# Kernel tuning notes

Hardware: AMD Instinct MI355X
Metric: run time of the kernel (lower is better)

The kernel has to match this reference:

```python
import jax, jax.numpy as jnp
from jax import lax
import numpy as np

D_MODEL = 256
NQ = 256          # nqueries / npoint
RADIUS = 0.3
NSAMPLE = 16
EPS = 1e-5


def _conv1d(x, W, b):  # x: (B,C,N), W: (O,C)
    return jnp.einsum('bcn,oc->bon', x, W) + b[None, :, None]


def _bn1d(x, g, be):  # train-mode batchnorm over (B, N)
    m = x.mean(axis=(0, 2), keepdims=True)
    v = x.var(axis=(0, 2), keepdims=True)
    return g[None, :, None] * (x - m) * lax.rsqrt(v + EPS) + be[None, :, None]


def _bn2d(x, g, be):  # x: (B,C,Q,S)
    m = x.mean(axis=(0, 2, 3), keepdims=True)
    v = x.var(axis=(0, 2, 3), keepdims=True)
    return g[None, :, None, None] * (x - m) * lax.rsqrt(v + EPS) + be[None, :, None, None]


def _fps(xyz, nq):
    # sequential farthest point sampling, starts at index 0 (matches CUDA impl)
    B, N, _ = xyz.shape

    def step(carry, _):
        dist, far = carry
        centroid = jnp.take_along_axis(xyz, far[:, None, None], axis=1)  # (B,1,3)
        d = jnp.sum((xyz - centroid) ** 2, axis=-1)                      # (B,N)
        dist = jnp.minimum(dist, d)
        nxt = jnp.argmax(dist, axis=-1).astype(jnp.int32)
        return (dist, nxt), far

    init = (jnp.full((B, N), 1e10, xyz.dtype), jnp.zeros((B,), jnp.int32))
    _, inds = lax.scan(step, init, None, length=nq)
    return inds.T  # (B,nq)


def _ball_query(query_xyz, xyz, radius, nsample):
    # query_xyz: (B,Q,3), xyz: (B,N,3) -> idx (B,Q,nsample) int32
    N = xyz.shape[1]
    d2 = jnp.sum((query_xyz[:, :, None, :] - xyz[:, None, :, :]) ** 2, axis=-1)  # (B,Q,N)
    within = d2 < radius * radius
    scores = jnp.where(within, jnp.arange(N, dtype=jnp.int32), jnp.int32(N))
    neg_top, _ = lax.top_k(-scores, nsample)          # nsample smallest scores, in order
    idx = -neg_top                                    # (B,Q,nsample)
    cnt = within.sum(axis=-1)                         # (B,Q)
    first = jnp.where(cnt > 0, idx[..., 0], 0)        # fill value (first neighbor, else 0)
    valid = jnp.arange(nsample) < cnt[..., None]
    return jnp.where(valid, idx, first[..., None])


def setup_inputs() -> dict:
    key = jax.random.key(0)
    ks = jax.random.split(key, 32)
    B, N, C = 16, 4096, D_MODEL
    s = 0.02
    inp = {
        'encode_xyz': jax.random.uniform(ks[0], (B, N, 3), jnp.float32),
        'encode_features': jax.random.normal(ks[1], (B, C, N), jnp.float32),
        # FFN_vote: conv1 -> bn -> relu -> conv2 -> bn -> relu -> conv3
        'W1': jax.random.normal(ks[2], (C, C), jnp.float32) * s,
        'b1': jnp.zeros((C,), jnp.float32),
        'g1': jnp.ones((C,), jnp.float32),
        'be1': jnp.zeros((C,), jnp.float32),
        'W2': jax.random.normal(ks[3], (C, C), jnp.float32) * s,
        'b2': jnp.zeros((C,), jnp.float32),
        'g2': jnp.ones((C,), jnp.float32),
        'be2': jnp.zeros((C,), jnp.float32),
        'W3': jax.random.normal(ks[4], (3 + C, C), jnp.float32) * s,
        'b3': jnp.zeros((3 + C,), jnp.float32),
        # SA module shared MLP (conv2d 1x1): (C+3)->C->C->C, each with BN2d
        'mW1': jax.random.normal(ks[5], (C, C + 3), jnp.float32) * s,
        'mb1': jnp.zeros((C,), jnp.float32),
        'mg1': jnp.ones((C,), jnp.float32),
        'mbe1': jnp.zeros((C,), jnp.float32),
        'mW2': jax.random.normal(ks[6], (C, C), jnp.float32) * s,
        'mb2': jnp.zeros((C,), jnp.float32),
        'mg2': jnp.ones((C,), jnp.float32),
        'mbe2': jnp.zeros((C,), jnp.float32),
        'mW3': jax.random.normal(ks[7], (C, C), jnp.float32) * s,
        'mb3': jnp.zeros((C,), jnp.float32),
        'mg3': jnp.ones((C,), jnp.float32),
        'mbe3': jnp.zeros((C,), jnp.float32),
    }
    return inp


def reference(encode_xyz, encode_features, W1, b1, g1, be1, W2, b2, g2, be2, W3, b3,
              mW1, mb1, mg1, mbe1, mW2, mb2, mg2, mbe2, mW3, mb3, mg3, mbe3):
    B, N, _ = encode_xyz.shape

    # FFN_vote
    h = jax.nn.relu(_bn1d(_conv1d(encode_features, W1, b1), g1, be1))
    h = jax.nn.relu(_bn1d(_conv1d(h, W2, b2), g2, be2))
    out = _conv1d(h, W3, b3)                      # (B, 3+C, N)

    coord_shift = jnp.clip(jax.nn.sigmoid(out[:, :3, :]), 0.1, 0.9)
    vote_xyz = encode_xyz + coord_shift.transpose(0, 2, 1) - 0.5   # (B,N,3)

    feat = encode_features + out[:, 3:, :]
    feat = feat / jnp.linalg.norm(feat, axis=1, keepdims=True)     # L2 normalize over C

    sample_inds = _fps(encode_xyz, NQ)                             # (B,NQ) int32

    # SA module: gather new centers from vote_xyz at FPS inds
    query_xyz = jnp.take_along_axis(vote_xyz, sample_inds[:, :, None], axis=1)  # (B,NQ,3)

    idx = _ball_query(query_xyz, vote_xyz, RADIUS, NSAMPLE)        # (B,NQ,NS)
    bidx = jnp.arange(B)[:, None, None]
    grouped_xyz = (vote_xyz[bidx, idx] - query_xyz[:, :, None, :]) / RADIUS  # (B,NQ,NS,3)
    grouped_feat = feat.transpose(0, 2, 1)[bidx, idx]                         # (B,NQ,NS,C)
    g = jnp.concatenate([grouped_xyz, grouped_feat], axis=-1)                 # (B,NQ,NS,3+C)
    g = g.transpose(0, 3, 1, 2)                                               # (B,3+C,NQ,NS)

    g = jax.nn.relu(_bn2d(jnp.einsum('bcqs,oc->boqs', g, mW1) + mb1[None, :, None, None], mg1, mbe1))
    g = jax.nn.relu(_bn2d(jnp.einsum('bcqs,oc->boqs', g, mW2) + mb2[None, :, None, None], mg2, mbe2))
    g = jax.nn.relu(_bn2d(jnp.einsum('bcqs,oc->boqs', g, mW3) + mb3[None, :, None, None], mg3, mbe3))
    query_features = jnp.max(g, axis=-1)                                      # (B,C,NQ)

    return vote_xyz, encode_xyz, sample_inds, query_xyz, query_features
```

## Files before the change

kernel.cpp:

```cpp
#include <hip/hip_runtime.h>
#include <math.h>

#define NPT 4096
#define NB 16

typedef short v8s __attribute__((ext_vector_type(8)));
typedef float v4f __attribute__((ext_vector_type(4)));

__device__ __forceinline__ float dist2e(float x, float y, float z,
                                        float cx, float cy, float cz) {
    float dx = __fsub_rn(x, cx), dy = __fsub_rn(y, cy), dz = __fsub_rn(z, cz);
    return __fadd_rn(__fadd_rn(__fmul_rn(dx, dx), __fmul_rn(dy, dy)), __fmul_rn(dz, dz));
}

__device__ __forceinline__ unsigned long long packdi(float v, int n) {
    return ((unsigned long long)__float_as_uint(v) << 32) |
           (unsigned long long)(0xFFFFFFFFu - (unsigned)n);
}

__device__ __forceinline__ unsigned short f2bf(float f) {
    unsigned u = __float_as_uint(f);
    u = u + 0x7FFFu + ((u >> 16) & 1u);
    return (unsigned short)(u >> 16);
}

__device__ __forceinline__ unsigned pk2(float a, float b) {
    unsigned r;
    asm("v_cvt_pk_bf16_f32 %0, %1, %2" : "=v"(r) : "v"(a), "v"(b));
    return r;
}

__device__ __forceinline__ uint2 split2(float a, float b) {
    unsigned h = pk2(a, b);
    float ra = __uint_as_float(h << 16);
    float rb = __uint_as_float(h & 0xFFFF0000u);
    unsigned l = pk2(a - ra, b - rb);
    return make_uint2(h, l);
}

__device__ __forceinline__ void bn8(v4f* xv, const float* __restrict__ scl,
                                    const float* __restrict__ sft, int base) {
    const v4f s0 = *(const v4f*)(scl + base);
    const v4f s1 = *(const v4f*)(scl + base + 4);
    const v4f f0 = *(const v4f*)(sft + base);
    const v4f f1 = *(const v4f*)(sft + base + 4);
    #pragma unroll
    for (int i = 0; i < 8; ++i) {
        const float si = (i < 4) ? s0[i] : s1[i - 4];
        const float fi = (i < 4) ? f0[i] : f1[i - 4];
        #pragma unroll
        for (int j = 0; j < 4; ++j)
            xv[i][j] = fmaxf(fmaf(xv[i][j], si, fi), 0.f);
    }
}

template <int CTRL>
__device__ __forceinline__ float dpp_maxf(float v) {
    int o = __builtin_amdgcn_update_dpp(__float_as_int(v), __float_as_int(v),
                                        CTRL, 0xF, 0xF, false);
    return fmaxf(v, __int_as_float(o));
}
template <int CTRL>
__device__ __forceinline__ unsigned dpp_maxu(unsigned v) {
    unsigned o = (unsigned)__builtin_amdgcn_update_dpp((int)v, (int)v,
                                                       CTRL, 0xF, 0xF, false);
    return v > o ? v : o;
}

__device__ void fps_seg(const float* __restrict__ xyz, int b, int it0, int it1,
                        int* __restrict__ inds_i, float* __restrict__ inds_f,
                        float* __restrict__ dws, int* __restrict__ farws,
                        char* scr) {
    unsigned long long (*s_red)[4] = (unsigned long long (*)[4])scr;
    const int t = threadIdx.x;
    const int lane = t & 63, wid = t >> 6;
    const float* pb = xyz + (size_t)b * NPT * 3;
    float px[16], py[16], pz[16], d[16];
    #pragma unroll
    for (int j = 0; j < 16; ++j) {
        int p = j * 256 + t;
        px[j] = pb[p * 3 + 0];
        py[j] = pb[p * 3 + 1];
        pz[j] = pb[p * 3 + 2];
    }
    int far;
    if (it0 == 0) {
        #pragma unroll
        for (int j = 0; j < 16; ++j) d[j] = 1e10f;
        far = 0;
    } else {
        #pragma unroll
        for (int j = 0; j < 16; ++j) d[j] = dws[b * 4096 + j * 256 + t];
        far = farws[b];
    }
    for (int it = it0; it < it1; ++it) {
        const int par = it & 1;
        if (t == 0) { inds_i[it] = far; inds_f[it] = (float)far; }
        const float cx = pb[far * 3 + 0];
        const float cy = pb[far * 3 + 1];
        const float cz = pb[far * 3 + 2];
        d[0] = fminf(d[0], dist2e(px[0], py[0], pz[0], cx, cy, cz));
        unsigned long long best = packdi(d[0], t);
        #pragma unroll
        for (int j = 1; j < 16; ++j) {
            d[j] = fminf(d[j], dist2e(px[j], py[j], pz[j], cx, cy, cz));
            unsigned long long c = packdi(d[j], j * 256 + t);
            if (c > best) best = c;
        }
        const unsigned hi = (unsigned)(best >> 32);
        const unsigned lo = (unsigned)(best & 0xFFFFFFFFull);
        float m = __uint_as_float(hi);
        m = dpp_maxf<0x111>(m);
        m = dpp_maxf<0x112>(m);
        m = dpp_maxf<0x114>(m);
        m = dpp_maxf<0x118>(m);
        m = dpp_maxf<0x142>(m);
        m = dpp_maxf<0x143>(m);
        const unsigned mbits = (unsigned)__builtin_amdgcn_readlane(__float_as_int(m), 63);
        unsigned cand = (hi == mbits) ? lo : 0u;
        cand = dpp_maxu<0x111>(cand);
        cand = dpp_maxu<0x112>(cand);
        cand = dpp_maxu<0x114>(cand);
        cand = dpp_maxu<0x118>(cand);
        cand = dpp_maxu<0x142>(cand);
        cand = dpp_maxu<0x143>(cand);
        const unsigned wlo = (unsigned)__builtin_amdgcn_readlane((int)cand, 63);
        if (lane == 0)
            s_red[par][wid] = ((unsigned long long)mbits << 32) | (unsigned long long)wlo;
        __syncthreads();
        unsigned long long mm = s_red[par][0];
        if (s_red[par][1] > mm) mm = s_red[par][1];
        if (s_red[par][2] > mm) mm = s_red[par][2];
        if (s_red[par][3] > mm) mm = s_red[par][3];
        far = (int)(0xFFFFFFFFu - (unsigned)(mm & 0xFFFFFFFFull));
    }
    if (it1 < 256) {
        #pragma unroll
        for (int j = 0; j < 16; ++j) dws[b * 4096 + j * 256 + t] = d[j];
        if (t == 0) farws[b] = far;
    }
}

template <bool PRE_BN, bool STATS>
__global__ __launch_bounds__(256, 4)
void fgemm_k(const float* __restrict__ X,
             const unsigned short* __restrict__ Wh,
             const unsigned short* __restrict__ Wl,
             const float* __restrict__ bias,
             const float* __restrict__ scl, const float* __restrict__ sft,
             float* __restrict__ Y,
             float* __restrict__ psum, float* __restrict__ psqr,
             const float* __restrict__ xyz, int* __restrict__ sinds,
             float* __restrict__ inds_f, float* __restrict__ fpsd,
             int* __restrict__ fpsfar, int it0, int it1) {
    __shared__ __align__(16) unsigned short sBh[128 * 64];
    __shared__ __align__(16) unsigned short sBl[128 * 64];
    if (blockIdx.x < 16) {
        fps_seg(xyz, blockIdx.x, it0, it1, sinds + blockIdx.x * 256,
                inds_f + blockIdx.x * 256, fpsd, fpsfar, (char*)sBh);
        return;
    }
    int idx = blockIdx.x - 16;
    idx = (idx & 7) * 128 + (idx >> 3);
    const int b = idx >> 6, rem = idx & 63;
    const int nt = rem >> 1;
    const int n0 = nt * 128, o0 = (rem & 1) * 128;
    const int t = threadIdx.x;
    const int w = t >> 6, lane = t & 63;
    const int wm = (w >> 1) * 64, wn = (w & 1) * 64;
    const int lr = lane & 15, lk = lane >> 4;
    char* cBh = (char*)sBh;
    char* cBl = (char*)sBl;

    v4f acc[4][4];
    v4f zz = {0.f, 0.f, 0.f, 0.f};
    #pragma unroll
    for (int i = 0; i < 4; ++i)
        #pragma unroll
        for (int j = 0; j < 4; ++j) acc[i][j] = zz;

    const size_t aoff = (size_t)(o0 + wm + lr) * 256 + lk * 8;
    const unsigned short* pah = Wh + aoff;
    const unsigned short* pal = Wl + aoff;

    const int cblk = t >> 5, nq = t & 31;
    const float* xb = X + ((size_t)b * 256 + cblk * 8) * 4096 + n0 + nq * 4;

    v4f cur[8];
    #pragma unroll
    for (int i = 0; i < 8; ++i)
        cur[i] = *(const v4f*)(xb + (size_t)i * 4096);
    if (PRE_BN) bn8(cur, scl, sft, cblk * 8);

    #pragma unroll
    for (int ks = 0; ks < 4; ++ks) {
        const int k0 = ks * 64;
        __syncthreads();
        #pragma unroll
        for (int j = 0; j < 4; ++j) {
            const int n = nq * 4 + j;
            uint2 p0 = split2(cur[0][j], cur[1][j]);
            uint2 p1 = split2(cur[2][j], cur[3][j]);
            uint2 p2 = split2(cur[4][j], cur[5][j]);
            uint2 p3 = split2(cur[6][j], cur[7][j]);
            uint4 hh, ll;
            hh.x = p0.x; hh.y = p1.x; hh.z = p2.x; hh.w = p3.x;
            ll.x = p0.y; ll.y = p1.y; ll.z = p2.y; ll.w = p3.y;
            const int ad = n * 128 + ((cblk * 16) ^ ((n & 7) << 4));
            *(uint4*)(cBh + ad) = hh;
            *(uint4*)(cBl + ad) = ll;
        }
        __syncthreads();
        if (ks < 3) {
            #pragma unroll
            for (int i = 0; i < 8; ++i)
                cur[i] = *(const v4f*)(xb + (size_t)(k0 + 64 + i) * 4096);
            if (PRE_BN) bn8(cur, scl, sft, k0 + 64 + cblk * 8);
        }
        #pragma unroll
        for (int kb = 0; kb < 2; ++kb) {
            const int koff = kb * 64 + lk * 16;
            const int ka = k0 + kb * 32;
            v8s ahf[4], alf[4], bhf[4], blf[4];
            #pragma unroll
            for (int f = 0; f < 4; ++f) {
                ahf[f] = *(const v8s*)(pah + (size_t)f * 4096 + ka);
                alf[f] = *(const v8s*)(pal + (size_t)f * 4096 + ka);
                const int rn = wn + f * 16 + lr;
                const int bm = rn * 128 + (koff ^ ((rn & 7) << 4));
                bhf[f] = *(const v8s*)(cBh + bm);
                blf[f] = *(const v8s*)(cBl + bm);
            }
            #pragma unroll
            for (int fm = 0; fm < 4; ++fm)
                #pragma unroll
                for (int fn = 0; fn < 4; ++fn) {
                    acc[fm][fn] = __builtin_amdgcn_mfma_f32_16x16x32_bf16(
                        ahf[fm], bhf[fn], acc[fm][fn], 0, 0, 0);
                    acc[fm][fn] = __builtin_amdgcn_mfma_f32_16x16x32_bf16(
                        ahf[fm], blf[fn], acc[fm][fn], 0, 0, 0);
                    acc[fm][fn] = __builtin_amdgcn_mfma_f32_16x16x32_bf16(
                        alf[fm], bhf[fn], acc[fm][fn], 0, 0, 0);
                }
        }
    }

    float* Yb = Y + (size_t)b * 256 * 4096;
    const int gnt = b * 32 + nt;
    #pragma unroll
    for (int fm = 0; fm < 4; ++fm) {
        const int obase = o0 + wm + fm * 16 + lk * 4;
        float bv[4];
        #pragma unroll
        for (int j = 0; j < 4; ++j) bv[j] = bias[obase + j];
        float ssr[4] = {0.f, 0.f, 0.f, 0.f}, qqr[4] = {0.f, 0.f, 0.f, 0.f};
        #pragma unroll
        for (int fn = 0; fn < 4; ++fn) {
            const int gn = n0 + wn + fn * 16 + lr;
            #pragma unroll
            for (int j = 0; j < 4; ++j) {
                const float yv = acc[fm][fn][j] + bv[j];
                Yb[(size_t)(obase + j) * 4096 + gn] = yv;
                ssr[j] += yv; qqr[j] += yv * yv;
            }
        }
        if (STATS) {
            #pragma unroll
            for (int j = 0; j < 4; ++j) {
                #pragma unroll
                for (int off = 1; off < 16; off <<= 1) {
                    ssr[j] += __shfl_xor(ssr[j], off, 64);
                    qqr[j] += __shfl_xor(qqr[j], off, 64);
                }
            }
            if (lr == 0) {
                const int col = gnt * 2 + (w & 1);
                #pragma unroll
                for (int j = 0; j < 4; ++j) {
                    psum[(size_t)(obase + j) * 1024 + col] = ssr[j];
                    psqr[(size_t)(obase + j) * 1024 + col] = qqr[j];
                }
            }
        }
    }
}

__global__ __launch_bounds__(256)
void prepw_k(const float* __restrict__ W1, const float* __restrict__ W2,
             const float* __restrict__ W3, unsigned short* __restrict__ h1,
             unsigned short* __restrict__ l1, unsigned short* __restrict__ h2,
             unsigned short* __restrict__ l2, unsigned short* __restrict__ h3,
             unsigned short* __restrict__ l3) {
    const int o = blockIdx.x & 255, which = blockIdx.x >> 8, t = threadIdx.x;
    float v;
    unsigned short* ph;
    unsigned short* pl;
    if (which == 0) { v = W1[(size_t)o * 256 + t]; ph = h1; pl = l1; }
    else if (which == 1) { v = W2[(size_t)o * 256 + t]; ph = h2; pl = l2; }
    else { v = W3[(size_t)(o + 3) * 256 + t]; ph = h3; pl = l3; }
    unsigned short hu = f2bf(v);
    float rv = v - __uint_as_float((unsigned)hu << 16);
    ph[o * 256 + t] = hu;
    pl[o * 256 + t] = f2bf(rv);
}

__global__ __launch_bounds__(64)
void fin_k(const float* __restrict__ psum, const float* __restrict__ psqr,
           const float* __restrict__ g, const float* __restrict__ be,
           float* __restrict__ scl, float* __restrict__ sft, int npart) {
    const int c = blockIdx.x, t = threadIdx.x;
    const float4* ps = (const float4*)(psum + (size_t)c * 1024);
    const float4* pq = (const float4*)(psqr + (size_t)c * 1024);
    float s = 0.f, q = 0.f;
    for (int r = t; r < (npart >> 2); r += 64) {
        float4 a = ps[r]; s += a.x + a.y + a.z + a.w;
        float4 b2 = pq[r]; q += b2.x + b2.y + b2.z + b2.w;
    }
    #pragma unroll
    for (int sh = 32; sh; sh >>= 1) {
        s += __shfl_down(s, (unsigned)sh, 64);
        q += __shfl_down(q, (unsigned)sh, 64);
    }
    if (t == 0) {
        float mean = s * (1.f / 65536.f);
        float var = q * (1.f / 65536.f) - mean * mean;
        float sc = g[c] / sqrtf(var + 1e-5f);
        scl[c] = sc;
        sft[c] = be[c] - mean * sc;
    }
}

__global__ __launch_bounds__(256)
void prep_k(const float* __restrict__ mW1, const float* __restrict__ mW2,
            const float* __restrict__ mW3, unsigned short* __restrict__ W1p,
            unsigned short* __restrict__ W2p, unsigned short* __restrict__ W3p) {
    const int o = blockIdx.x & 255, which = blockIdx.x >> 8, t = threadIdx.x;
    if (which == 0) {
        W1p[o * 320 + t] = f2bf(mW1[o * 259 + 3 + t]);
        if (t < 64) {
            float v = (t < 3) ? mW1[o * 259 + t] : 0.f;
            W1p[o * 320 + 256 + t] = f2bf(v);
        }
    } else if (which == 1) {
        W2p[o * 256 + t] = f2bf(mW2[o * 256 + t]);
    } else {
        W3p[o * 256 + t] = f2bf(mW3[o * 256 + t]);
    }
}

__global__ __launch_bounds__(256)
void votefeat_k(const float* __restrict__ OUT, const float* __restrict__ Y2,
                const float* __restrict__ xyz, const float* __restrict__ feats,
                const float* __restrict__ scl2, const float* __restrict__ sft2,
                const float* __restrict__ W3, const float* __restrict__ b3,
                float* __restrict__ vote_out, float* __restrict__ xyz_out,
                unsigned short* __restrict__ featT,
                int* __restrict__ sinds, float* __restrict__ inds_f,
                float* __restrict__ fpsd, int* __restrict__ fpsfar,
                int it0, int it1) {
    __shared__ float tile[32 * 257];
    __shared__ float ssb[32 * 9];
    __shared__ float rn[32];
    __shared__ float sW3[768];
    __shared__ float dred[3][8][33];
    if (blockIdx.x < 16) {
        fps_seg(xyz, blockIdx.x, it0, it1, sinds + blockIdx.x * 256,
                inds_f + blockIdx.x * 256, fpsd, fpsfar, (char*)tile);
        return;
    }
    const int blk = blockIdx.x - 16;
    const int b = blk >> 7, n0 = (blk & 127) * 32;
    const int t = threadIdx.x;
    const int nl = t & 31, co = t >> 5;
    const float* Ob = OUT + (size_t)b * 256 * NPT;
    const float* Yb = Y2 + (size_t)b * 256 * NPT;
    #pragma unroll
    for (int r = 0; r < 3; ++r) sW3[r * 256 + t] = W3[r * 256 + t];
    __syncthreads();
    float ss = 0.f, d0 = 0.f, d1 = 0.f, d2 = 0.f;
    #pragma unroll 4
    for (int ci = 0; ci < 32; ++ci) {
        const int c = ci * 8 + co;
        const size_t coff = (size_t)c * NPT + n0 + nl;
        float v = feats[(size_t)b * 256 * NPT + coff] + Ob[coff];
        tile[nl * 257 + c] = v;
        ss += v * v;
        float h = fmaxf(fmaf(Yb[coff], scl2[c], sft2[c]), 0.f);
        d0 = fmaf(h, sW3[c], d0);
        d1 = fmaf(h, sW3[256 + c], d1);
        d2 = fmaf(h, sW3[512 + c], d2);
    }
    ssb[nl * 9 + co] = ss;
    dred[0][co][nl] = d0;
    dred[1][co][nl] = d1;
    dred[2][co][nl] = d2;
    __syncthreads();
    if (t < 32) {
        float s = 0.f;
        #pragma unroll
        for (int j = 0; j < 8; ++j) s += ssb[t * 9 + j];
        rn[t] = 1.0f / sqrtf(s);
    }
    __syncthreads();
    for (int p = 0; p < 32; ++p)
        featT[((size_t)b * NPT + n0 + p) * 256 + t] = f2bf(tile[p * 257 + t] * rn[p]);
    if (t < 96) {
        const int r = t >> 5, p = t & 31;
        float d = b3[r];
        #pragma unroll
        for (int j = 0; j < 8; ++j) d += dred[r][j][p];
        float sig = 1.f / (1.f + expf(-d));
        sig = fminf(fmaxf(sig, 0.1f), 0.9f);
        const size_t gi = ((size_t)b * NPT + n0 + p) * 3 + r;
        const float e = xyz[gi];
        vote_out[gi] = e + sig - 0.5f;
        xyz_out[gi] = e;
    }
}

__global__ __launch_bounds__(64)
void bq_k(const float* __restrict__ vote, const int* __restrict__ sinds,
          float* __restrict__ qxyz_out, int* __restrict__ idx_out) {
    const int bq = blockIdx.x;
    const int b = bq >> 8;
    const int lane = threadIdx.x;
    __shared__ int s_idx[16];
    const int si = sinds[bq];
    const float* vb = vote + (size_t)b * NPT * 3;
    const float qx = vb[si * 3 + 0], qy = vb[si * 3 + 1], qz = vb[si * 3 + 2];
    if (lane < 3) qxyz_out[bq * 3 + lane] = vb[si * 3 + lane];
    int cnt = 0;
    for (int cb = 0; cb < 64 && cnt < 16; ++cb) {
        int n = cb * 64 + lane;
        float x = vb[n * 3], y = vb[n * 3 + 1], z = vb[n * 3 + 2];
        float d2 = dist2e(x, y, z, qx, qy, qz);
        unsigned long long m = __ballot(d2 < 0.09f);
        while (m && cnt < 16) {
            int bit = __builtin_ctzll(m);
            s_idx[cnt] = cb * 64 + bit;
            ++cnt;
            m &= m - 1;
        }
    }
    __syncthreads();
    if (lane < 16) {
        int v = (lane < cnt) ? s_idx[lane] : (cnt > 0 ? s_idx[0] : 0);
        idx_out[bq * 16 + lane] = v;
    }
}

__global__ __launch_bounds__(256)
void group_k(const unsigned short* __restrict__ featT, const float* __restrict__ vote,
             const float* __restrict__ qxyz, const int* __restrict__ idxs,
             unsigned short* __restrict__ Gt) {
    const int bq = blockIdx.x;
    const int b = bq >> 8, q = bq & 255;
    const int t = threadIdx.x;
    __shared__ int s_i[16];
    __shared__ float s_q[3];
    if (t < 16) s_i[t] = idxs[bq * 16 + t];
    if (t < 3) s_q[t] = qxyz[bq * 3 + t];
    __syncthreads();
    const int s = t >> 4, part = t & 15;
    const int i = s_i[s];
    const size_t nrow = (size_t)b * 4096 + q * 16 + s;
    const uint4* src = (const uint4*)(featT + ((size_t)b * NPT + i) * 256 + part * 16);
    uint4* dst = (uint4*)(Gt + nrow * 320 + part * 16);
    dst[0] = src[0];
    dst[1] = src[1];
    for (int c = 259 + part; c < 320; c += 16) Gt[nrow * 320 + c] = 0;
    if (part < 3) {
        float v = (vote[((size_t)b * NPT + i) * 3 + part] - s_q[part]) * (1.f / 0.3f);
        Gt[nrow * 320 + 256 + part] = f2bf(v);
    }
}

__device__ __forceinline__ unsigned bnpair(unsigned u, float sl, float sh,
                                           float fl, float fh) {
    float lo = __uint_as_float(u << 16);
    float hi = __uint_as_float(u & 0xFFFF0000u);
    lo = fmaxf(fmaf(lo, sl, fl), 0.f);
    hi = fmaxf(fmaf(hi, sh, fh), 0.f);
    unsigned r;
    asm("v_cvt_pk_bf16_f32 %0, %1, %2" : "=v"(r) : "v"(lo), "v"(hi));
    return r;
}

template <int KPAD, bool BNSTAGE, bool EPIMAX>
__global__ __launch_bounds__(256, 2)
void mgemm_k(const unsigned short* __restrict__ Wb,
             const unsigned short* __restrict__ Xt,
             const float* __restrict__ bias,
             const float* __restrict__ scl, const float* __restrict__ sft,
             unsigned short* __restrict__ Yt, float* __restrict__ rmax,
             float* __restrict__ psum, float* __restrict__ psqr) {
    __shared__ __align__(16) unsigned short sA[128 * 64];
    __shared__ __align__(16) unsigned short sB[128 * 64];
    char* cA = (char*)sA;
    char* cB = (char*)sB;
    const int t = threadIdx.x;
    const int n0 = blockIdx.x * 128, o0 = blockIdx.y * 128;
    const int w = t >> 6, lane = t & 63;
    const int wm = (w >> 1) * 64, wn = (w & 1) * 64;
    const int lr = lane & 15, lk = lane >> 4;

    v4f acc[4][4];
    v4f zz = {0.f, 0.f, 0.f, 0.f};
    #pragma unroll
    for (int i = 0; i < 4; ++i)
        #pragma unroll
        for (int j = 0; j < 4; ++j) acc[i][j] = zz;

    const int ra = t >> 1, kc = (t & 1) * 32;
    const unsigned short* asrc = Wb + (size_t)(o0 + ra) * KPAD + kc;
    const unsigned short* bsrc = Xt + (size_t)(n0 + ra) * KPAD + kc;
    constexpr int nk = KPAD / 64;

    uint4 av[4], bv[4];
    #pragma unroll
    for (int i = 0; i < 4; ++i) av[i] = *(const uint4*)(asrc + 8 * i);
    #pragma unroll
    for (int i = 0; i < 4; ++i) bv[i] = *(const uint4*)(bsrc + 8 * i);
    if constexpr (BNSTAGE) {
        #pragma unroll
        for (int i = 0; i < 4; ++i) {
            const int kk = kc + 8 * i;
            float4 s0 = *(const float4*)(scl + kk);
            float4 s1 = *(const float4*)(scl + kk + 4);
            float4 f0 = *(const float4*)(sft + kk);
            float4 f1 = *(const float4*)(sft + kk + 4);
            bv[i].x = bnpair(bv[i].x, s0.x, s0.y, f0.x, f0.y);
            bv[i].y = bnpair(bv[i].y, s0.z, s0.w, f0.z, f0.w);
            bv[i].z = bnpair(bv[i].z, s1.x, s1.y, f1.x, f1.y);
            bv[i].w = bnpair(bv[i].w, s1.z, s1.w, f1.z, f1.w);
        }
    }

    #pragma unroll
    for (int ks = 0; ks < nk; ++ks) {
        __syncthreads();
        #pragma unroll
        for (int i = 0; i < 4; ++i) {
            const int kb2 = (kc + 8 * i) * 2;
            *(uint4*)(cA + ra * 128 + (kb2 ^ ((ra & 7) << 4))) = av[i];
            *(uint4*)(cB + ra * 128 + (kb2 ^ ((ra & 7) << 4))) = bv[i];
        }
        __syncthreads();
        if (ks + 1 < nk) {
            const int k1 = (ks + 1) * 64;
            #pragma unroll
            for (int i = 0; i < 4; ++i) av[i] = *(const uint4*)(asrc + k1 + 8 * i);
            #pragma unroll
            for (int i = 0; i < 4; ++i) bv[i] = *(const uint4*)(bsrc + k1 + 8 * i);
            if constexpr (BNSTAGE) {
                #pragma unroll
                for (int i = 0; i < 4; ++i) {
                    const int kk = k1 + kc + 8 * i;
                    float4 s0 = *(const float4*)(scl + kk);
                    float4 s1 = *(const float4*)(scl + kk + 4);
                    float4 f0 = *(const float4*)(sft + kk);
                    float4 f1 = *(const float4*)(sft + kk + 4);
                    bv[i].x = bnpair(bv[i].x, s0.x, s0.y, f0.x, f0.y);
                    bv[i].y = bnpair(bv[i].y, s0.z, s0.w, f0.z, f0.w);
                    bv[i].z = bnpair(bv[i].z, s1.x, s1.y, f1.x, f1.y);
                    bv[i].w = bnpair(bv[i].w, s1.z, s1.w, f1.z, f1.w);
                }
            }
        }
        #pragma unroll
        for (int kb = 0; kb < 2; ++kb) {
            const int koff = (kb * 32 + lk * 8) * 2;
            v8s af[4], bf[4];
            #pragma unroll
            for (int f = 0; f < 4; ++f) {
                const int rm = wm + f * 16 + lr;
                af[f] = *(const v8s*)(cA + rm * 128 + (koff ^ ((rm & 7) << 4)));
                const int rn = wn + f * 16 + lr;
                bf[f] = *(const v8s*)(cB + rn * 128 + (koff ^ ((rn & 7) << 4)));
            }
            #pragma unroll
            for (int fm = 0; fm < 4; ++fm)
                #pragma unroll
                for (int fn = 0; fn < 4; ++fn)
                    acc[fm][fn] = __builtin_amdgcn_mfma_f32_16x16x32_bf16(
                        af[fm], bf[fn], acc[fm][fn], 0, 0, 0);
        }
    }

    const int bx = blockIdx.x;
    #pragma unroll
    for (int fm = 0; fm < 4; ++fm) {
        const int obase = o0 + wm + fm * 16 + lk * 4;
        const float4 bv4 = *(const float4*)(bias + obase);
        float s0 = 0.f, s1 = 0.f, s2 = 0.f, s3 = 0.f;
        float q0 = 0.f, q1 = 0.f, q2 = 0.f, q3 = 0.f;
        #pragma unroll
        for (int fn = 0; fn < 4; ++fn) {
            float y0 = acc[fm][fn][0] + bv4.x;
            float y1 = acc[fm][fn][1] + bv4.y;
            float y2 = acc[fm][fn][2] + bv4.z;
            float y3 = acc[fm][fn][3] + bv4.w;
            s0 += y0; s1 += y1; s2 += y2; s3 += y3;
            q0 += y0 * y0; q1 += y1 * y1; q2 += y2 * y2; q3 += y3 * y3;
            if constexpr (!EPIMAX) {
                unsigned p0, p1;
                asm("v_cvt_pk_bf16_f32 %0, %1, %2" : "=v"(p0) : "v"(y0), "v"(y1));
                asm("v_cvt_pk_bf16_f32 %0, %1, %2" : "=v"(p1) : "v"(y2), "v"(y3));
                const int gn = n0 + wn + fn * 16 + lr;
                *(uint2*)(Yt + (size_t)gn * 256 + obase) = make_uint2(p0, p1);
            } else {
                float m0 = y0, m1 = y1, m2 = y2, m3 = y3;
                #pragma unroll
                for (int off = 1; off < 16; off <<= 1) {
                    m0 = fmaxf(m0, __shfl_xor(m0, off, 64));
                    m1 = fmaxf(m1, __shfl_xor(m1, off, 64));
                    m2 = fmaxf(m2, __shfl_xor(m2, off, 64));
                    m3 = fmaxf(m3, __shfl_xor(m3, off, 64));
                }
                if (lr == 0) {
                    const int gq = (n0 + wn + fn * 16) >> 4;
                    const int bb = gq >> 8, qq = gq & 255;
                    float* rp = rmax + ((size_t)bb * 256 + obase) * 256 + qq;
                    rp[0] = m0; rp[256] = m1; rp[512] = m2; rp[768] = m3;
                }
            }
        }
        #pragma unroll
        for (int off = 1; off < 16; off <<= 1) {
            s0 += __shfl_xor(s0, off, 64); q0 += __shfl_xor(q0, off, 64);
            s1 += __shfl_xor(s1, off, 64); q1 += __shfl_xor(q1, off, 64);
            s2 += __shfl_xor(s2, off, 64); q2 += __shfl_xor(q2, off, 64);
            s3 += __shfl_xor(s3, off, 64); q3 += __shfl_xor(q3, off, 64);
        }
        if (lr == 0) {
            const int col = bx * 2 + (w & 1);
            psum[(size_t)(obase + 0) * 1024 + col] = s0;
            psum[(size_t)(obase + 1) * 1024 + col] = s1;
            psum[(size_t)(obase + 2) * 1024 + col] = s2;
            psum[(size_t)(obase + 3) * 1024 + col] = s3;
            psqr[(size_t)(obase + 0) * 1024 + col] = q0;
            psqr[(size_t)(obase + 1) * 1024 + col] = q1;
            psqr[(size_t)(obase + 2) * 1024 + col] = q2;
            psqr[(size_t)(obase + 3) * 1024 + col] = q3;
        }
    }
}

__global__ __launch_bounds__(256)
void qf_k(const float* __restrict__ rmax, const float* __restrict__ scl,
          const float* __restrict__ sft, float* __restrict__ out) {
    const int g = blockIdx.x * 256 + threadIdx.x;
    const int c = (g >> 8) & 255;
    out[g] = fmaxf(fmaf(rmax[g], scl[c], sft[c]), 0.f);
}

extern "C" void kernel_launch(void* const* d_in, const int* in_sizes, int n_in,
                              void* d_out, int out_size, void* d_ws, size_t ws_size,
                              hipStream_t stream) {
    const float* xyz   = (const float*)d_in[0];
    const float* feats = (const float*)d_in[1];
    const float* W1 = (const float*)d_in[2];
    const float* b1 = (const float*)d_in[3];
    const float* g1 = (const float*)d_in[4];
    const float* be1 = (const float*)d_in[5];
    const float* W2 = (const float*)d_in[6];
    const float* b2 = (const float*)d_in[7];
    const float* g2 = (const float*)d_in[8];
    const float* be2 = (const float*)d_in[9];
    const float* W3 = (const float*)d_in[10];
    const float* b3 = (const float*)d_in[11];
    const float* mW1 = (const float*)d_in[12];
    const float* mb1 = (const float*)d_in[13];
    const float* mg1 = (const float*)d_in[14];
    const float* mbe1 = (const float*)d_in[15];
    const float* mW2 = (const float*)d_in[16];
    const float* mb2 = (const float*)d_in[17];
    const float* mg2 = (const float*)d_in[18];
    const float* mbe2 = (const float*)d_in[19];
    const float* mW3 = (const float*)d_in[20];
    const float* mb3 = (const float*)d_in[21];
    const float* mg3 = (const float*)d_in[22];
    const float* mbe3 = (const float*)d_in[23];

    float* out_vote = (float*)d_out;
    float* out_xyz = out_vote + 196608;
    float* out_inds = out_xyz + 196608;
    float* out_q = out_inds + 4096;
    float* out_qf = out_q + 12288;

    float* ws = (float*)d_ws;
    float* A      = ws;
    float* Bb     = A + 16973824;
    float* Ft     = Bb + 16777216;
    float* rawmax = Ft + 8388608;
    float* psum   = rawmax + 1048576;
    float* psqr   = psum + 262144;
    float* st     = psqr + 262144;
    float* fpsd   = st + 2560;
    float* wbase  = fpsd + 65536;
    unsigned short* Wb1 = (unsigned short*)wbase;
    unsigned short* Wb2 = Wb1 + 81920;
    unsigned short* Wb3 = Wb2 + 65536;
    int* sinds  = (int*)(Wb3 + 65536);
    int* bidx   = sinds + 4096;
    int* fpsfar = bidx + 65536;

    unsigned short* Gt  = (unsigned short*)A;
    unsigned short* Y1t = (unsigned short*)Bb;
    unsigned short* featT = (unsigned short*)Ft;
    unsigned short* Y2t = (unsigned short*)Ft;

    unsigned short* Wf1h = (unsigned short*)rawmax;
    unsigned short* Wf1l = Wf1h + 65536;
    unsigned short* Wf2h = Wf1l + 65536;
    unsigned short* Wf2l = Wf2h + 65536;
    unsigned short* Wf3h = Wf2l + 65536;
    unsigned short* Wf3l = Wf3h + 65536;

    prep_k<<<768, 256, 0, stream>>>(mW1, mW2, mW3, Wb1, Wb2, Wb3);
    prepw_k<<<768, 256, 0, stream>>>(W1, W2, W3, Wf1h, Wf1l, Wf2h, Wf2l, Wf3h, Wf3l);

    fgemm_k<false, true><<<1040, 256, 0, stream>>>(
        feats, Wf1h, Wf1l, b1, nullptr, nullptr, A, psum, psqr,
        xyz, sinds, out_inds, fpsd, fpsfar, 0, 64);
    fin_k<<<256, 64, 0, stream>>>(psum, psqr, g1, be1, st + 0, st + 256, 1024);
    fgemm_k<true, true><<<1040, 256, 0, stream>>>(
        A, Wf2h, Wf2l, b2, st + 0, st + 256, Bb, psum, psqr,
        xyz, sinds, out_inds, fpsd, fpsfar, 64, 128);
    fin_k<<<256, 64, 0, stream>>>(psum, psqr, g2, be2, st + 512, st + 768, 1024);
    fgemm_k<true, false><<<1040, 256, 0, stream>>>(
        Bb, Wf3h, Wf3l, b3 + 3, st + 512, st + 768, A, nullptr, nullptr,
        xyz, sinds, out_inds, fpsd, fpsfar, 128, 192);

    votefeat_k<<<2064, 256, 0, stream>>>(A, Bb, xyz, feats, st + 512, st + 768,
                                         W3, b3, out_vote, out_xyz, featT,
                                         sinds, out_inds, fpsd, fpsfar, 192, 256);
    bq_k<<<4096, 64, 0, stream>>>(out_vote, sinds, out_q, bidx);
    group_k<<<4096, 256, 0, stream>>>(featT, out_vote, out_q, bidx, Gt);

    mgemm_k<320, false, false><<<dim3(512, 2), 256, 0, stream>>>(
        Wb1, Gt, mb1, nullptr, nullptr, Y1t, nullptr, psum, psqr);
    fin_k<<<256, 64, 0, stream>>>(psum, psqr, mg1, mbe1, st + 1024, st + 1280, 1024);
    mgemm_k<256, true, false><<<dim3(512, 2), 256, 0, stream>>>(
        Wb2, Y1t, mb2, st + 1024, st + 1280, Y2t, nullptr, psum, psqr);
    fin_k<<<256, 64, 0, stream>>>(psum, psqr, mg2, mbe2, st + 1536, st + 1792, 1024);
    mgemm_k<256, true, true><<<dim3(512, 2), 256, 0, stream>>>(
        Wb3, Y2t, mb3, st + 1536, st + 1792, nullptr, rawmax, psum, psqr);
    fin_k<<<256, 64, 0, stream>>>(psum, psqr, mg3, mbe3, st + 2048, st + 2304, 1024);
    qf_k<<<4096, 256, 0, stream>>>(rawmax, st + 2048, st + 2304, out_qf);
}
```

Baseline: 565.3 us.

## Vectorize votefeat loads and stores, read GEMM weights directly from global memory

The votefeat kernel now has each thread load 4 consecutive points per channel with vector loads. It reduces partial sums over 32 slices and writes featT as packed bf16 pairs through 8-byte stores. The MFMA GEMM no longer stages the weight tile in shared memory; each lane loads its A fragments straight from global memory (weights are small and cache-resident), halving LDS use and raising launch bounds occupancy to 4 blocks. This trades LDS traffic and syncs for more global/L2 loads on the A operand and relies on a pk2 helper presumed defined elsewhere.

Measured after the change: 554.1 us. 1.02x faster.

```diff
diff --git a/kernel.cpp b/kernel.cpp
--- a/kernel.cpp
+++ b/kernel.cpp
@@ -359,10 +359,10 @@
                 float* __restrict__ fpsd, int* __restrict__ fpsfar,
                 int it0, int it1) {
     __shared__ float tile[32 * 257];
-    __shared__ float ssb[32 * 9];
+    __shared__ float ssb[32][33];
     __shared__ float rn[32];
     __shared__ float sW3[768];
-    __shared__ float dred[3][8][33];
+    __shared__ float dred[3][32][33];
     if (blockIdx.x < 16) {
         fps_seg(xyz, blockIdx.x, it0, it1, sinds + blockIdx.x * 256,
                 inds_f + blockIdx.x * 256, fpsd, fpsfar, (char*)tile);
@@ -371,44 +371,70 @@
     const int blk = blockIdx.x - 16;
     const int b = blk >> 7, n0 = (blk & 127) * 32;
     const int t = threadIdx.x;
-    const int nl = t & 31, co = t >> 5;
+    const int nl4 = (t & 7) * 4, sl = t >> 3;
+    const float* Fb = feats + (size_t)b * 256 * NPT;
     const float* Ob = OUT + (size_t)b * 256 * NPT;
     const float* Yb = Y2 + (size_t)b * 256 * NPT;
     #pragma unroll
     for (int r = 0; r < 3; ++r) sW3[r * 256 + t] = W3[r * 256 + t];
     __syncthreads();
-    float ss = 0.f, d0 = 0.f, d1 = 0.f, d2 = 0.f;
-    #pragma unroll 4
-    for (int ci = 0; ci < 32; ++ci) {
-        const int c = ci * 8 + co;
-        const size_t coff = (size_t)c * NPT + n0 + nl;
-        float v = feats[(size_t)b * 256 * NPT + coff] + Ob[coff];
-        tile[nl * 257 + c] = v;
-        ss += v * v;
-        float h = fmaxf(fmaf(Yb[coff], scl2[c], sft2[c]), 0.f);
-        d0 = fmaf(h, sW3[c], d0);
-        d1 = fmaf(h, sW3[256 + c], d1);
-        d2 = fmaf(h, sW3[512 + c], d2);
-    }
-    ssb[nl * 9 + co] = ss;
-    dred[0][co][nl] = d0;
-    dred[1][co][nl] = d1;
-    dred[2][co][nl] = d2;
+    float ss[4] = {0.f, 0.f, 0.f, 0.f};
+    float dd[3][4];
+    #pragma unroll
+    for (int r = 0; r < 3; ++r)
+        #pragma unroll
+        for (int j = 0; j < 4; ++j) dd[r][j] = 0.f;
+    #pragma unroll
+    for (int ci = 0; ci < 8; ++ci) {
+        const int c = ci * 32 + sl;
+        const size_t coff = (size_t)c * NPT + n0 + nl4;
+        const v4f f4 = *(const v4f*)(Fb + coff);
+        const v4f o4 = *(const v4f*)(Ob + coff);
+        const v4f y4 = *(const v4f*)(Yb + coff);
+        const float s2 = scl2[c], sh2 = sft2[c];
+        const float w0 = sW3[c], w1 = sW3[256 + c], w2 = sW3[512 + c];
+        #pragma unroll
+        for (int j = 0; j < 4; ++j) {
+            const float v = f4[j] + o4[j];
+            tile[(nl4 + j) * 257 + c] = v;
+            ss[j] = fmaf(v, v, ss[j]);
+            const float h = fmaxf(fmaf(y4[j], s2, sh2), 0.f);
+            dd[0][j] = fmaf(h, w0, dd[0][j]);
+            dd[1][j] = fmaf(h, w1, dd[1][j]);
+            dd[2][j] = fmaf(h, w2, dd[2][j]);
+        }
+    }
+    #pragma unroll
+    for (int j = 0; j < 4; ++j) ssb[nl4 + j][sl] = ss[j];
+    #pragma unroll
+    for (int r = 0; r < 3; ++r)
+        #pragma unroll
+        for (int j = 0; j < 4; ++j) dred[r][nl4 + j][sl] = dd[r][j];
     __syncthreads();
     if (t < 32) {
         float s = 0.f;
         #pragma unroll
-        for (int j = 0; j < 8; ++j) s += ssb[t * 9 + j];
+        for (int k = 0; k < 32; ++k) s += ssb[t][k];
         rn[t] = 1.0f / sqrtf(s);
     }
     __syncthreads();
-    for (int p = 0; p < 32; ++p)
-        featT[((size_t)b * NPT + n0 + p) * 256 + t] = f2bf(tile[p * 257 + t] * rn[p]);
+    #pragma unroll
+    for (int pp = 0; pp < 8; ++pp) {
+        const int p = pp * 4 + (t >> 6);
+        const int ch = (t & 63) * 4;
+        const float rv = rn[p];
+        const float v0 = tile[p * 257 + ch + 0] * rv;
+        const float v1 = tile[p * 257 + ch + 1] * rv;
+        const float v2 = tile[p * 257 + ch + 2] * rv;
+        const float v3 = tile[p * 257 + ch + 3] * rv;
+        *(uint2*)&featT[((size_t)b * NPT + n0 + p) * 256 + ch] =
+            make_uint2(pk2(v0, v1), pk2(v2, v3));
+    }
     if (t < 96) {
         const int r = t >> 5, p = t & 31;
         float d = b3[r];
         #pragma unroll
-        for (int j = 0; j < 8; ++j) d += dred[r][j][p];
+        for (int k = 0; k < 32; ++k) d += dred[r][p][k];
         float sig = 1.f / (1.f + expf(-d));
         sig = fminf(fmaxf(sig, 0.1f), 0.9f);
         const size_t gi = ((size_t)b * NPT + n0 + p) * 3 + r;
@@ -487,16 +513,14 @@
 }
 
 template <int KPAD, bool BNSTAGE, bool EPIMAX>
-__global__ __launch_bounds__(256, 2)
+__global__ __launch_bounds__(256, 4)
 void mgemm_k(const unsigned short* __restrict__ Wb,
              const unsigned short* __restrict__ Xt,
              const float* __restrict__ bias,
              const float* __restrict__ scl, const float* __restrict__ sft,
              unsigned short* __restrict__ Yt, float* __restrict__ rmax,
              float* __restrict__ psum, float* __restrict__ psqr) {
-    __shared__ __align__(16) unsigned short sA[128 * 64];
     __shared__ __align__(16) unsigned short sB[128 * 64];
-    char* cA = (char*)sA;
     char* cB = (char*)sB;
     const int t = threadIdx.x;
     const int n0 = blockIdx.x * 128, o0 = blockIdx.y * 128;
@@ -511,14 +535,13 @@
         #pragma unroll
         for (int j = 0; j < 4; ++j) acc[i][j] = zz;
 
+    const unsigned short* pa = Wb + (size_t)(o0 + wm + lr) * KPAD + lk * 8;
+
     const int ra = t >> 1, kc = (t & 1) * 32;
-    const unsigned short* asrc = Wb + (size_t)(o0 + ra) * KPAD + kc;
     const unsigned short* bsrc = Xt + (size_t)(n0 + ra) * KPAD + kc;
     constexpr int nk = KPAD / 64;
 
-    uint4 av[4], bv[4];
-    #pragma unroll
-    for (int i = 0; i < 4; ++i) av[i] = *(const uint4*)(asrc + 8 * i);
+    uint4 bv[4];
     #pragma unroll
     for (int i = 0; i < 4; ++i) bv[i] = *(const uint4*)(bsrc + 8 * i);
     if constexpr (BNSTAGE) {
@@ -542,14 +565,11 @@
         #pragma unroll
         for (int i = 0; i < 4; ++i) {
             const int kb2 = (kc + 8 * i) * 2;
-            *(uint4*)(cA + ra * 128 + (kb2 ^ ((ra & 7) << 4))) = av[i];
             *(uint4*)(cB + ra * 128 + (kb2 ^ ((ra & 7) << 4))) = bv[i];
         }
         __syncthreads();
         if (ks + 1 < nk) {
             const int k1 = (ks + 1) * 64;
-            #pragma unroll
-            for (int i = 0; i < 4; ++i) av[i] = *(const uint4*)(asrc + k1 + 8 * i);
             #pragma unroll
             for (int i = 0; i < 4; ++i) bv[i] = *(const uint4*)(bsrc + k1 + 8 * i);
             if constexpr (BNSTAGE) {
@@ -570,11 +590,11 @@
         #pragma unroll
         for (int kb = 0; kb < 2; ++kb) {
             const int koff = (kb * 32 + lk * 8) * 2;
+            const int ka = ks * 64 + kb * 32;
             v8s af[4], bf[4];
             #pragma unroll
             for (int f = 0; f < 4; ++f) {
-                const int rm = wm + f * 16 + lr;
-                af[f] = *(const v8s*)(cA + rm * 128 + (koff ^ ((rm & 7) << 4)));
+                af[f] = *(const v8s*)(pa + (size_t)(f * 16) * KPAD + ka);
                 const int rn = wn + f * 16 + lr;
                 bf[f] = *(const v8s*)(cB + rn * 128 + (koff ^ ((rn & 7) << 4)));
             }
```
